# Kernel tuning notes

Hardware: AMD Instinct MI355X
Metric: run time of the kernel (lower is better)

## Reference

```python
import jax, jax.numpy as jnp
import numpy as np

ALPHA = 0.2

def _ema_last_weights(T, alpha, dtype):
    # Closed form for the final EMA value after the sequential recurrence:
    # ema_T = (1-a)^(T-1) * x_0 + sum_{t=1}^{T-1} a*(1-a)^(T-1-t) * x_t
    t = jnp.arange(T)
    w = alpha * (1.0 - alpha) ** (T - 1 - t)
    w = w.at[0].set((1.0 - alpha) ** (T - 1))
    return w.astype(dtype)


def setup_inputs() -> dict:
    key = jax.random.key(0)
    k1, k2 = jax.random.split(key)
    B, T, F = 64, 2048, 256
    x = jax.random.normal(k1, (B, T, F), dtype=jnp.float32)
    W = jax.random.normal(k2, (F, F), dtype=jnp.float32) * (1.0 / np.sqrt(F))
    b = jnp.zeros((F,), dtype=jnp.float32)
    return {"x": x, "W": W, "b": b}


def reference(x, W, b):
    B, T, F = x.shape
    # final-step EMA over time (equivalent to the sequential python loop)
    w = _ema_last_weights(T, ALPHA, x.dtype)          # [T]
    last_ref = jnp.einsum('t,btf->bf', w, x)[:, None, :]  # [B,1,F]
    # base residual predictor: per-timestep linear
    res = jnp.einsum('btf,fg->btg', x, W) + b          # [B,T,F]
    return last_ref + res
```

## Files before the change

kernel.cpp:

```cpp
#include <hip/hip_runtime.h>

#define Bdim 64
#define Tdim 2048
#define Fdim 256
#define TAIL 256
#define NCH 8
#define CHT 32

#define BM 64
#define BK 32
#define NCHUNK 8

typedef __bf16 bf16x8 __attribute__((ext_vector_type(8)));
typedef float f32x16 __attribute__((ext_vector_type(16)));
typedef unsigned short u16x8 __attribute__((ext_vector_type(8)));

__device__ __forceinline__ unsigned short bf16_rne(float f) {
  unsigned int u = __float_as_uint(f);
  u += 0x7FFFu + ((u >> 16) & 1u);
  return (unsigned short)(u >> 16);
}

__global__ void prep(const float* __restrict__ x, const float* __restrict__ W,
                     unsigned short* __restrict__ Wf, float* __restrict__ part) {
  int blk = blockIdx.x;
  if (blk < Fdim) {
    int o = blk * 256 + threadIdx.x;
    int e = o & 7, lane = (o >> 3) & 63, wh = (o >> 9) & 1, s = (o >> 10) & 1;
    int c = (o >> 11) & 7, w = o >> 14;
    int n = w * 64 + wh * 32 + (lane & 31);
    int k = c * 32 + (2 * s + (lane >> 5)) * 8 + e;
    Wf[o] = bf16_rne(W[k * Fdim + n]);
  } else {
    int j = blk - Fdim;
    int b = j & 63, c = j >> 6;
    int f = threadIdx.x;
    int t0 = Tdim - TAIL + c * CHT;
    float w = 0.2f * exp2f((float)(Tdim - 1 - t0) * -0.32192809488736235f);
    const float* xp = x + ((size_t)b * Tdim + t0) * Fdim + f;
    float s = 0.f;
#pragma unroll
    for (int q = 0; q < CHT; ++q) {
      s += w * xp[(size_t)q * Fdim];
      w *= 1.25f;
    }
    part[(c * Bdim + b) * Fdim + f] = s;
  }
}

__global__ __launch_bounds__(256, 4)
void gemm_fused(const float* __restrict__ x, const unsigned short* __restrict__ Wf,
                const float* __restrict__ bias, const float* __restrict__ part,
                float* __restrict__ out) {
  __shared__ unsigned short Abuf[2][4 * 64 * 8];
  __shared__ float lref[Fdim];

  const int tid = threadIdx.x;
  const int blk = blockIdx.x;
  const int b = blk >> 5;
  const size_t row0 = (size_t)blk * BM;

  const int wave = tid >> 6;
  const int lane = tid & 63;
  const int lm = lane & 31;
  const int half = lane >> 5;

  {
    float s = bias[tid];
#pragma unroll
    for (int c = 0; c < NCH; ++c) s += part[(c * Bdim + b) * Fdim + tid];
    lref[tid] = s;
  }

  const int srow = (wave >> 1) * 32 + lm;
  const int scol = ((wave & 1) * 2 + half) * 8;
  const float* asrc = x + (row0 + srow) * Fdim + scol;
  const int adst = tid * 8;

  const unsigned short* bsrc = Wf + (size_t)wave * (32 * 512) + lane * 8;

  f32x16 acc[2][2] = {};
  float4 Ar[2][2];
  bf16x8 Bf[2][2];

  Ar[0][0] = *(const float4*)asrc;
  Ar[0][1] = *(const float4*)(asrc + 4);
  Bf[0][0] = *(const bf16x8*)(bsrc + 0 * 512);
  Bf[0][1] = *(const bf16x8*)(bsrc + 1 * 512);
  Bf[1][0] = *(const bf16x8*)(bsrc + 2 * 512);
  Bf[1][1] = *(const bf16x8*)(bsrc + 3 * 512);
  {
    float4 v0 = Ar[0][0], v1 = Ar[0][1];
    u16x8 w;
    w[0] = bf16_rne(v0.x); w[1] = bf16_rne(v0.y);
    w[2] = bf16_rne(v0.z); w[3] = bf16_rne(v0.w);
    w[4] = bf16_rne(v1.x); w[5] = bf16_rne(v1.y);
    w[6] = bf16_rne(v1.z); w[7] = bf16_rne(v1.w);
    *(u16x8*)&Abuf[0][adst] = w;
  }
  Ar[1][0] = *(const float4*)(asrc + BK);
  Ar[1][1] = *(const float4*)(asrc + BK + 4);
  __syncthreads();

#pragma unroll
  for (int c = 0; c < NCHUNK; ++c) {
    const int cur = c & 1, nxt = cur ^ 1;
    if (c + 2 < NCHUNK) {
      const float* s4 = asrc + (c + 2) * BK;
      Ar[cur][0] = *(const float4*)s4;
      Ar[cur][1] = *(const float4*)(s4 + 4);
    }
#pragma unroll
    for (int s = 0; s < 2; ++s) {
      bf16x8 a0 = *(const bf16x8*)&Abuf[cur][(s * 64 + lane) * 8];
      bf16x8 a1 = *(const bf16x8*)&Abuf[cur][((2 + s) * 64 + lane) * 8];
      acc[0][0] = __builtin_amdgcn_mfma_f32_32x32x16_bf16(a0, Bf[s][0], acc[0][0], 0, 0, 0);
      acc[0][1] = __builtin_amdgcn_mfma_f32_32x32x16_bf16(a0, Bf[s][1], acc[0][1], 0, 0, 0);
      acc[1][0] = __builtin_amdgcn_mfma_f32_32x32x16_bf16(a1, Bf[s][0], acc[1][0], 0, 0, 0);
      acc[1][1] = __builtin_amdgcn_mfma_f32_32x32x16_bf16(a1, Bf[s][1], acc[1][1], 0, 0, 0);
      if (c + 1 < NCHUNK) {
        const unsigned short* bs = bsrc + (c + 1) * (4 * 512) + s * 1024;
        Bf[s][0] = *(const bf16x8*)bs;
        Bf[s][1] = *(const bf16x8*)(bs + 512);
      }
    }
    if (c + 1 < NCHUNK) {
      float4 v0 = Ar[nxt][0], v1 = Ar[nxt][1];
      u16x8 w;
      w[0] = bf16_rne(v0.x); w[1] = bf16_rne(v0.y);
      w[2] = bf16_rne(v0.z); w[3] = bf16_rne(v0.w);
      w[4] = bf16_rne(v1.x); w[5] = bf16_rne(v1.y);
      w[6] = bf16_rne(v1.z); w[7] = bf16_rne(v1.w);
      *(u16x8*)&Abuf[nxt][adst] = w;
      __syncthreads();
    }
  }

  float* op = out + row0 * Fdim;
  const int rbase = 4 * half;
#pragma unroll
  for (int i = 0; i < 2; ++i) {
#pragma unroll
    for (int j = 0; j < 2; ++j) {
      int n = wave * 64 + j * 32 + lm;
      float lb = lref[n];
#pragma unroll
      for (int r = 0; r < 16; ++r) {
        int rowi = i * 32 + (r & 3) + 8 * (r >> 2) + rbase;
        op[(size_t)rowi * Fdim + n] = acc[i][j][r] + lb;
      }
    }
  }
}

extern "C" void kernel_launch(void* const* d_in, const int* in_sizes, int n_in,
                              void* d_out, int out_size, void* d_ws, size_t ws_size,
                              hipStream_t stream) {
  const float* x = (const float*)d_in[0];
  const float* W = (const float*)d_in[1];
  const float* bias = (const float*)d_in[2];
  float* out = (float*)d_out;

  unsigned short* Wf = (unsigned short*)d_ws;
  float* part = (float*)((char*)d_ws + Fdim * Fdim * sizeof(unsigned short));

  prep<<<Fdim + Bdim * NCH, 256, 0, stream>>>(x, W, Wf, part);
  gemm_fused<<<(Bdim * Tdim) / BM, 256, 0, stream>>>(x, Wf, bias, part, out);
}
```

Baseline: 247.0 us.

## Load A operands directly into registers, drop LDS staging and per-chunk barriers

Each wave now loads its own 32-row A slice straight from global memory into registers and converts it to bf16 there, so the shared-memory A buffer and the per-chunk __syncthreads are gone. The wave tiling changes from 2x2 32x32 tiles per wave to a 1x4 layout (32 rows x 128 columns), and the W fragment layout in prep is reordered to match. The aim is to remove LDS traffic and barrier stalls. In exchange, A loads are duplicated across the two N-waves and register pressure rises, so the launch bound drops to 3 blocks per SIMD.

Result: slower. 285.7 us (+15.7%).

```diff
diff --git a/kernel.cpp b/kernel.cpp
--- a/kernel.cpp
+++ b/kernel.cpp
@@ -7,9 +7,9 @@
 #define NCH 8
 #define CHT 32
 
-#define BM 64
 #define BK 32
 #define NCHUNK 8
+#define PFD 2
 
 typedef __bf16 bf16x8 __attribute__((ext_vector_type(8)));
 typedef float f32x16 __attribute__((ext_vector_type(16)));
@@ -26,9 +26,9 @@
   int blk = blockIdx.x;
   if (blk < Fdim) {
     int o = blk * 256 + threadIdx.x;
-    int e = o & 7, lane = (o >> 3) & 63, wh = (o >> 9) & 1, s = (o >> 10) & 1;
-    int c = (o >> 11) & 7, w = o >> 14;
-    int n = w * 64 + wh * 32 + (lane & 31);
+    int e = o & 7, lane = (o >> 3) & 63, nsub = (o >> 9) & 7, s = (o >> 12) & 1;
+    int c = o >> 13;
+    int n = nsub * 32 + (lane & 31);
     int k = c * 32 + (2 * s + (lane >> 5)) * 8 + e;
     Wf[o] = bf16_rne(W[k * Fdim + n]);
   } else {
@@ -48,19 +48,20 @@
   }
 }
 
-__global__ __launch_bounds__(256, 4)
+__global__ __launch_bounds__(256, 3)
 void gemm_fused(const float* __restrict__ x, const unsigned short* __restrict__ Wf,
                 const float* __restrict__ bias, const float* __restrict__ part,
                 float* __restrict__ out) {
-  __shared__ unsigned short Abuf[2][4 * 64 * 8];
   __shared__ float lref[Fdim];
 
   const int tid = threadIdx.x;
   const int blk = blockIdx.x;
   const int b = blk >> 5;
-  const size_t row0 = (size_t)blk * BM;
+  const size_t row0 = (size_t)blk * 64;
 
   const int wave = tid >> 6;
+  const int mw = wave >> 1;
+  const int nw = wave & 1;
   const int lane = tid & 63;
   const int lm = lane & 31;
   const int half = lane >> 5;
@@ -71,84 +72,72 @@
     for (int c = 0; c < NCH; ++c) s += part[(c * Bdim + b) * Fdim + tid];
     lref[tid] = s;
   }
+  __syncthreads();
 
-  const int srow = (wave >> 1) * 32 + lm;
-  const int scol = ((wave & 1) * 2 + half) * 8;
-  const float* asrc = x + (row0 + srow) * Fdim + scol;
-  const int adst = tid * 8;
+  const float* ax = x + (row0 + mw * 32 + lm) * Fdim;
+  const unsigned short* bx = Wf + (size_t)(nw * 4) * 512 + lane * 8;
 
-  const unsigned short* bsrc = Wf + (size_t)wave * (32 * 512) + lane * 8;
+  f32x16 acc[4] = {};
+  float4 Ar[PFD][2][2];
+  bf16x8 Bf[2][4];
 
-  f32x16 acc[2][2] = {};
-  float4 Ar[2][2];
-  bf16x8 Bf[2][2];
-
-  Ar[0][0] = *(const float4*)asrc;
-  Ar[0][1] = *(const float4*)(asrc + 4);
-  Bf[0][0] = *(const bf16x8*)(bsrc + 0 * 512);
-  Bf[0][1] = *(const bf16x8*)(bsrc + 1 * 512);
-  Bf[1][0] = *(const bf16x8*)(bsrc + 2 * 512);
-  Bf[1][1] = *(const bf16x8*)(bsrc + 3 * 512);
-  {
-    float4 v0 = Ar[0][0], v1 = Ar[0][1];
-    u16x8 w;
-    w[0] = bf16_rne(v0.x); w[1] = bf16_rne(v0.y);
-    w[2] = bf16_rne(v0.z); w[3] = bf16_rne(v0.w);
-    w[4] = bf16_rne(v1.x); w[5] = bf16_rne(v1.y);
-    w[6] = bf16_rne(v1.z); w[7] = bf16_rne(v1.w);
-    *(u16x8*)&Abuf[0][adst] = w;
+#pragma unroll
+  for (int p = 0; p < PFD; ++p) {
+#pragma unroll
+    for (int s = 0; s < 2; ++s) {
+      const float* sp = ax + p * BK + (2 * s + half) * 8;
+      Ar[p][s][0] = *(const float4*)sp;
+      Ar[p][s][1] = *(const float4*)(sp + 4);
+    }
   }
-  Ar[1][0] = *(const float4*)(asrc + BK);
-  Ar[1][1] = *(const float4*)(asrc + BK + 4);
-  __syncthreads();
+#pragma unroll
+  for (int s = 0; s < 2; ++s)
+#pragma unroll
+    for (int j = 0; j < 4; ++j)
+      Bf[s][j] = *(const bf16x8*)(bx + (size_t)(s * 8 + j) * 512);
 
 #pragma unroll
   for (int c = 0; c < NCHUNK; ++c) {
-    const int cur = c & 1, nxt = cur ^ 1;
-    if (c + 2 < NCHUNK) {
-      const float* s4 = asrc + (c + 2) * BK;
-      Ar[cur][0] = *(const float4*)s4;
-      Ar[cur][1] = *(const float4*)(s4 + 4);
-    }
+    const int slot = c % PFD;
 #pragma unroll
     for (int s = 0; s < 2; ++s) {
-      bf16x8 a0 = *(const bf16x8*)&Abuf[cur][(s * 64 + lane) * 8];
-      bf16x8 a1 = *(const bf16x8*)&Abuf[cur][((2 + s) * 64 + lane) * 8];
-      acc[0][0] = __builtin_amdgcn_mfma_f32_32x32x16_bf16(a0, Bf[s][0], acc[0][0], 0, 0, 0);
-      acc[0][1] = __builtin_amdgcn_mfma_f32_32x32x16_bf16(a0, Bf[s][1], acc[0][1], 0, 0, 0);
-      acc[1][0] = __builtin_amdgcn_mfma_f32_32x32x16_bf16(a1, Bf[s][0], acc[1][0], 0, 0, 0);
-      acc[1][1] = __builtin_amdgcn_mfma_f32_32x32x16_bf16(a1, Bf[s][1], acc[1][1], 0, 0, 0);
-      if (c + 1 < NCHUNK) {
-        const unsigned short* bs = bsrc + (c + 1) * (4 * 512) + s * 1024;
-        Bf[s][0] = *(const bf16x8*)bs;
-        Bf[s][1] = *(const bf16x8*)(bs + 512);
-      }
-    }
-    if (c + 1 < NCHUNK) {
-      float4 v0 = Ar[nxt][0], v1 = Ar[nxt][1];
+      float4 v0 = Ar[slot][s][0], v1 = Ar[slot][s][1];
       u16x8 w;
       w[0] = bf16_rne(v0.x); w[1] = bf16_rne(v0.y);
       w[2] = bf16_rne(v0.z); w[3] = bf16_rne(v0.w);
       w[4] = bf16_rne(v1.x); w[5] = bf16_rne(v1.y);
       w[6] = bf16_rne(v1.z); w[7] = bf16_rne(v1.w);
-      *(u16x8*)&Abuf[nxt][adst] = w;
-      __syncthreads();
+      bf16x8 af;
+      *(u16x8*)&af = w;
+      acc[0] = __builtin_amdgcn_mfma_f32_32x32x16_bf16(af, Bf[s][0], acc[0], 0, 0, 0);
+      acc[1] = __builtin_amdgcn_mfma_f32_32x32x16_bf16(af, Bf[s][1], acc[1], 0, 0, 0);
+      acc[2] = __builtin_amdgcn_mfma_f32_32x32x16_bf16(af, Bf[s][2], acc[2], 0, 0, 0);
+      acc[3] = __builtin_amdgcn_mfma_f32_32x32x16_bf16(af, Bf[s][3], acc[3], 0, 0, 0);
+      if (c + 1 < NCHUNK) {
+#pragma unroll
+        for (int j = 0; j < 4; ++j)
+          Bf[s][j] = *(const bf16x8*)(bx + (size_t)(((c + 1) * 2 + s) * 8 + j) * 512);
+      }
+    }
+    if (c + PFD < NCHUNK) {
+#pragma unroll
+      for (int s = 0; s < 2; ++s) {
+        const float* sp = ax + (c + PFD) * BK + (2 * s + half) * 8;
+        Ar[slot][s][0] = *(const float4*)sp;
+        Ar[slot][s][1] = *(const float4*)(sp + 4);
+      }
     }
   }
 
-  float* op = out + row0 * Fdim;
+  float* op = out + (row0 + mw * 32) * Fdim + nw * 128;
   const int rbase = 4 * half;
 #pragma unroll
-  for (int i = 0; i < 2; ++i) {
+  for (int j = 0; j < 4; ++j) {
+    float lb = lref[nw * 128 + j * 32 + lm];
 #pragma unroll
-    for (int j = 0; j < 2; ++j) {
-      int n = wave * 64 + j * 32 + lm;
-      float lb = lref[n];
-#pragma unroll
-      for (int r = 0; r < 16; ++r) {
-        int rowi = i * 32 + (r & 3) + 8 * (r >> 2) + rbase;
-        op[(size_t)rowi * Fdim + n] = acc[i][j][r] + lb;
-      }
+    for (int r = 0; r < 16; ++r) {
+      int rowi = (r & 3) + 8 * (r >> 2) + rbase;
+      op[(size_t)rowi * Fdim + j * 32 + lm] = acc[j][r] + lb;
     }
   }
 }
@@ -165,5 +154,5 @@
   float* part = (float*)((char*)d_ws + Fdim * Fdim * sizeof(unsigned short));
 
   prep<<<Fdim + Bdim * NCH, 256, 0, stream>>>(x, W, Wf, part);
-  gemm_fused<<<(Bdim * Tdim) / BM, 256, 0, stream>>>(x, Wf, bias, part, out);
+  gemm_fused<<<(Bdim * Tdim) / 64, 256, 0, stream>>>(x, Wf, bias, part, out);
 }
```
